# Optimization experiments

Measured on AMD Instinct MI355X. Metric: run time of the kernel, lower is better.

Reference implementation:

```python
import jax, jax.numpy as jnp
import numpy as np

N_NODES = 100000
N_EDGES = 1600000
IN_FEATS = 128
HEADS = 4
OUT_FEATS = 16
NEG_SLOPE = 0.2  # DGL GATConv default negative_slope


def setup_inputs() -> dict:
    key = jax.random.key(0)
    ks = jax.random.split(key, 7)
    feats = jax.random.normal(ks[0], (N_NODES, IN_FEATS), dtype=jnp.float32)
    W = jax.random.normal(ks[1], (HEADS * OUT_FEATS, IN_FEATS), dtype=jnp.float32) * 0.05
    attn_l = jax.random.normal(ks[2], (HEADS, OUT_FEATS), dtype=jnp.float32) * 0.1
    attn_r = jax.random.normal(ks[3], (HEADS, OUT_FEATS), dtype=jnp.float32) * 0.1
    bias = jax.random.normal(ks[4], (HEADS * OUT_FEATS,), dtype=jnp.float32) * 0.01
    src = jax.random.randint(ks[5], (N_EDGES,), 0, N_NODES, dtype=jnp.int64 if jax.config.jax_enable_x64 else jnp.int32)
    dst = jax.random.randint(ks[6], (N_EDGES,), 0, N_NODES, dtype=jnp.int64 if jax.config.jax_enable_x64 else jnp.int32)
    return {"feats": feats, "W": W, "attn_l": attn_l, "attn_r": attn_r,
            "bias": bias, "src": src, "dst": dst}


def reference(feats, W, attn_l, attn_r, bias, src, dst):
    """GATConv forward on a homogeneous graph built from concatenated edge lists.

    feats: [N, in_feats]; W: [H*F, in_feats]; attn_l/attn_r: [H, F]; bias: [H*F]
    src/dst: [E] edge endpoint indices. Returns [N, H, F] (DGL GATConv output).
    """
    N = feats.shape[0]
    H, F = attn_l.shape
    # Linear projection, per-head split: z [N, H, F]
    z = (feats @ W.T).reshape(N, H, F)
    # Per-node attention logits: el/er [N, H]
    el = jnp.einsum('nhf,hf->nh', z, attn_l)
    er = jnp.einsum('nhf,hf->nh', z, attn_r)
    # Per-edge unnormalized attention: e [E, H]
    e = jax.nn.leaky_relu(el[src] + er[dst], negative_slope=NEG_SLOPE)
    # Edge softmax over incoming edges of each destination node
    m = jax.ops.segment_max(e, dst, num_segments=N)           # [N, H]
    m = jnp.where(jnp.isfinite(m), m, jnp.zeros_like(m))      # guard empty segments
    ex = jnp.exp(e - m[dst])                                  # [E, H]
    denom = jax.ops.segment_sum(ex, dst, num_segments=N)      # [N, H]
    alpha = ex / denom[dst]                                   # [E, H]
    # Weighted message aggregation: scatter-add z[src] * alpha into dst
    msg = z[src] * alpha[:, :, None]                          # [E, H, F]
    out = jax.ops.segment_sum(msg, dst, num_segments=N)       # [N, H, F]
    return out + bias.reshape(1, H, F)
```

## Files before the change

### kernel.cpp

```cpp
#include <hip/hip_runtime.h>

#define N_NODES 100000
#define N_EDGES 1600000
#define IN_F    128
#define HEADS   4
#define OUT_F   16
#define HF      64
#define NEG_SLOPE 0.2f

#define BUCK    112
#define NBUCK   893
#define BSTRIDE 2048

#define BSC_CHUNK 4096
#define NB_BSC5 391

#define NB_MFMA2 782
#define NB_FUSED5 1173

typedef __attribute__((ext_vector_type(8))) short short8;
typedef __attribute__((ext_vector_type(4))) float f32x4;

__device__ __forceinline__ short f2bf(float f) {
    union { float f; unsigned u; } v; v.f = f;
    return (short)((v.u + 0x7FFFu + ((v.u >> 16) & 1u)) >> 16);
}

__global__ __launch_bounds__(256) void k_prep(const float* __restrict__ W,
                                              const float* __restrict__ attn_l,
                                              const float* __restrict__ attn_r,
                                              unsigned short* __restrict__ Wfrag,
                                              int* __restrict__ gcur) {
    const int g = blockIdx.x, t = threadIdx.x;
    if (g >= 20) {
        int i = (g - 20) * 256 + t;
        if (i < 1024) gcur[i] = 0;
        return;
    }
    const int ct = g >> 2, kf = g & 3;
    #pragma unroll
    for (int e = 0; e < 2; ++e) {
        int off = e * 256 + t;
        int j = off & 7, lane = off >> 3;
        int n = lane & 15, qq = lane >> 4;
        int k = kf * 32 + qq * 8 + j;
        float v;
        if (ct < 4) {
            v = W[(size_t)(ct * 16 + n) * IN_F + k];
        } else if (n < 8) {
            int hh = n & 3;
            const float* at = (n < 4) ? attn_l : attn_r;
            v = 0.f;
            #pragma unroll
            for (int f = 0; f < 16; ++f)
                v += W[(size_t)(hh * 16 + f) * IN_F + k] * at[hh * 16 + f];
        } else {
            v = 0.f;
        }
        Wfrag[(size_t)g * 512 + off] = (unsigned short)f2bf(v);
    }
}

__global__ __launch_bounds__(512) void k_fused(const float* __restrict__ feats,
                                               const unsigned short* __restrict__ Wfrag,
                                               unsigned short* __restrict__ zb,
                                               float* __restrict__ el,
                                               float* __restrict__ er,
                                               const int* __restrict__ src,
                                               const int* __restrict__ dst,
                                               int* __restrict__ gcur,
                                               unsigned* __restrict__ bin) {
    const int t = threadIdx.x;
    const unsigned bx = blockIdx.x;
    const unsigned q3 = bx / 3u, r3 = bx % 3u;

    if (r3 == 0u) {
        __shared__ unsigned sortedL[BSC_CHUNK];
        __shared__ int hist[NBUCK];
        __shared__ int cur[NBUCK];

        const int bid = (int)q3;
        const int start = bid * BSC_CHUNK;
        int end = start + BSC_CHUNK;
        if (end > N_EDGES) end = N_EDGES;

        for (int i = t; i < NBUCK; i += 512) hist[i] = 0;
        __syncthreads();

        unsigned myv[8];
        #pragma unroll
        for (int k = 0; k < 8; ++k) {
            int i = start + t + k * 512;
            if (i < end) {
                unsigned d = (unsigned)dst[i];
                unsigned b = d / BUCK;
                myv[k] = (b << 7) | (d - b * BUCK);
                atomicAdd(&hist[b], 1);
            } else myv[k] = 0xFFFFFFFFu;
        }
        __syncthreads();

        if (t < 64) {
            int base = t * 14;
            int loc[14]; int acc = 0;
            #pragma unroll
            for (int k = 0; k < 14; ++k) {
                int idx = base + k;
                int v = (idx < NBUCK) ? hist[idx] : 0;
                loc[k] = acc; acc += v;
            }
            int x = acc;
            #pragma unroll
            for (int o = 1; o < 64; o <<= 1) {
                int y = __shfl_up(x, o);
                if (t >= o) x += y;
            }
            int excl = x - acc;
            #pragma unroll
            for (int k = 0; k < 14; ++k) {
                int idx = base + k;
                if (idx < NBUCK) cur[idx] = excl + loc[k];
            }
        }
        __syncthreads();

        #pragma unroll
        for (int k = 0; k < 8; ++k) {
            if (myv[k] != 0xFFFFFFFFu) {
                int i = start + t + k * 512;
                unsigned b = myv[k] >> 7;
                unsigned dl = myv[k] & 127u;
                int pos = atomicAdd(&cur[b], 1);
                sortedL[pos] = (unsigned)src[i] | (dl << 17);
            }
        }
        __syncthreads();

        for (int b = t; b < NBUCK; b += 512) {
            int n = hist[b];
            if (!n) continue;
            int lo = cur[b] - n;
            int gb = atomicAdd(&gcur[b], n);
            unsigned* dp = bin + (size_t)b * BSTRIDE;
            for (int k2 = 0; k2 < n; ++k2) {
                int gpos = gb + k2;
                if (gpos < BSTRIDE) dp[gpos] = sortedL[lo + k2];
            }
        }
        return;
    }

    const int bid = (int)(q3 * 2u + (r3 - 1u));

    const int grp = t >> 6;
    const int l = t & 63;
    const int q = l >> 4, n = l & 15;

    short8 bfrag[5][4];
    #pragma unroll
    for (int ct = 0; ct < 5; ++ct)
        #pragma unroll
        for (int kf = 0; kf < 4; ++kf)
            bfrag[ct][kf] = *(const short8*)(Wfrag + (size_t)((ct * 4 + kf) * 64 + l) * 8);

    int anode = bid * 128 + grp * 16 + n;
    int aclamp = anode < N_NODES ? anode : 0;
    const float* arow = feats + (size_t)aclamp * IN_F + q * 8;

    f32x4 acc[5];
    #pragma unroll
    for (int ct = 0; ct < 5; ++ct) acc[ct] = (f32x4){0.f, 0.f, 0.f, 0.f};

    #pragma unroll
    for (int kf = 0; kf < 4; ++kf) {
        float4 x = *(const float4*)(arow + kf * 32);
        float4 y = *(const float4*)(arow + kf * 32 + 4);
        short8 a;
        a[0] = f2bf(x.x); a[1] = f2bf(x.y); a[2] = f2bf(x.z); a[3] = f2bf(x.w);
        a[4] = f2bf(y.x); a[5] = f2bf(y.y); a[6] = f2bf(y.z); a[7] = f2bf(y.w);
        #pragma unroll
        for (int ct = 0; ct < 5; ++ct)
            acc[ct] = __builtin_amdgcn_mfma_f32_16x16x32_bf16(a, bfrag[ct][kf], acc[ct], 0, 0, 0);
    }

    #pragma unroll
    for (int reg = 0; reg < 4; ++reg) {
        int onode = bid * 128 + grp * 16 + q * 4 + reg;
        if (onode >= N_NODES) continue;
        #pragma unroll
        for (int ct = 0; ct < 4; ++ct)
            zb[(size_t)onode * HF + ct * 16 + n] = (unsigned short)f2bf(acc[ct][reg]);
        float v4 = acc[4][reg];
        if (n < 4)       el[onode * HEADS + n] = v4;
        else if (n < 8)  er[onode * HEADS + (n - 4)] = v4;
    }
}

__global__ __launch_bounds__(512) void k3_sort(const unsigned* __restrict__ bin,
                                               const int* __restrict__ gcur,
                                               const float* __restrict__ el,
                                               const float* __restrict__ er,
                                               const unsigned short* __restrict__ zb,
                                               const float* __restrict__ bias,
                                               float* __restrict__ out) {
    __shared__ unsigned raw[BSTRIDE];
    __shared__ unsigned sorted[BSTRIDE];
    __shared__ int hist[BUCK];
    __shared__ int noff[BUCK + 1];
    __shared__ int cur[BUCK];
    __shared__ int s[128];
    __shared__ float er_s[BUCK * HEADS];

    const int t = threadIdx.x;
    const int B = blockIdx.x;
    const int nodebase = B * BUCK;
    const unsigned* mybin = bin + (size_t)B * BSTRIDE;
    int cnt = gcur[B];
    if (cnt > BSTRIDE) cnt = BSTRIDE;

    if (t < BUCK) hist[t] = 0;
    if (t < BUCK * HEADS) {
        int g = nodebase * HEADS + t;
        er_s[t] = (g < N_NODES * HEADS) ? er[g] : 0.f;
    }
    for (int i = t; i < cnt; i += 512) raw[i] = mybin[i];
    __syncthreads();

    for (int i = t; i < cnt; i += 512)
        atomicAdd(&hist[raw[i] >> 17], 1);
    __syncthreads();

    if (t < 128) s[t] = (t < BUCK) ? hist[t] : 0;
    __syncthreads();
    for (int o = 1; o < 128; o <<= 1) {
        int x = (t < 128 && t >= o) ? s[t - o] : 0;
        __syncthreads();
        if (t < 128) s[t] += x;
        __syncthreads();
    }
    if (t < BUCK) {
        int excl = s[t] - hist[t];
        noff[t] = excl;
        cur[t] = excl;
    }
    if (t == 0) noff[BUCK] = s[BUCK - 1];
    __syncthreads();

    for (int i = t; i < cnt; i += 512) {
        unsigned p = raw[i];
        int pos = atomicAdd(&cur[p >> 17], 1);
        sorted[pos] = p & 0x1FFFF;
    }
    __syncthreads();

    const int wave = t >> 6, lane = t & 63;
    const int j = lane >> 3;
    const int c = lane & 7;
    const int h = c >> 1;
    const int jj = j & 3;
    const int sel = j >> 2;

    for (int p = wave; p < BUCK / 2; p += 8) {
        const int nl = p * 2 + sel;
        const int node = nodebase + nl;
        const int nlo = noff[nl], nhi = noff[nl + 1];
        const float er_d = er_s[nl * HEADS + h];

        float4 A0 = make_float4(0.f, 0.f, 0.f, 0.f);
        float4 A1 = make_float4(0.f, 0.f, 0.f, 0.f);
        float den = 0.f;
        for (int i = nlo + jj; i < nhi; i += 4) {
            int sN = (int)sorted[i];
            float x = el[sN * HEADS + h] + er_d;
            x = x > 0.f ? x : NEG_SLOPE * x;
            float ex = __expf(x);
            den += ex;
            uint4 v = *(const uint4*)(zb + (size_t)sN * HF + c * 8);
            A0.x += ex * __uint_as_float(v.x << 16);
            A0.y += ex * __uint_as_float(v.x & 0xFFFF0000u);
            A0.z += ex * __uint_as_float(v.y << 16);
            A0.w += ex * __uint_as_float(v.y & 0xFFFF0000u);
            A1.x += ex * __uint_as_float(v.z << 16);
            A1.y += ex * __uint_as_float(v.z & 0xFFFF0000u);
            A1.z += ex * __uint_as_float(v.w << 16);
            A1.w += ex * __uint_as_float(v.w & 0xFFFF0000u);
        }
        #pragma unroll
        for (int m = 8; m <= 16; m <<= 1) {
            A0.x += __shfl_xor(A0.x, m); A0.y += __shfl_xor(A0.y, m);
            A0.z += __shfl_xor(A0.z, m); A0.w += __shfl_xor(A0.w, m);
            A1.x += __shfl_xor(A1.x, m); A1.y += __shfl_xor(A1.y, m);
            A1.z += __shfl_xor(A1.z, m); A1.w += __shfl_xor(A1.w, m);
            den  += __shfl_xor(den,  m);
        }
        if (jj == 0 && node < N_NODES) {
            float4 b0 = *(const float4*)(bias + c * 8);
            float4 b1 = *(const float4*)(bias + c * 8 + 4);
            if (den > 0.f) {
                float inv = 1.f / den;
                b0.x += A0.x * inv; b0.y += A0.y * inv;
                b0.z += A0.z * inv; b0.w += A0.w * inv;
                b1.x += A1.x * inv; b1.y += A1.y * inv;
                b1.z += A1.z * inv; b1.w += A1.w * inv;
            }
            *(float4*)(out + (size_t)node * HF + c * 8) = b0;
            *(float4*)(out + (size_t)node * HF + c * 8 + 4) = b1;
        }
    }
}

extern "C" void kernel_launch(void* const* d_in, const int* in_sizes, int n_in,
                              void* d_out, int out_size, void* d_ws, size_t ws_size,
                              hipStream_t stream) {
    const float* feats  = (const float*)d_in[0];
    const float* W      = (const float*)d_in[1];
    const float* attn_l = (const float*)d_in[2];
    const float* attn_r = (const float*)d_in[3];
    const float* bias   = (const float*)d_in[4];
    const int*   src    = (const int*)d_in[5];
    const int*   dst    = (const int*)d_in[6];
    float* out = (float*)d_out;

    char* ws = (char*)d_ws;
    unsigned short* zb = (unsigned short*)ws;  ws += (size_t)N_NODES * HF * 2;
    float* el    = (float*)ws;                 ws += N_NODES * HEADS * 4;
    float* er    = (float*)ws;                 ws += N_NODES * HEADS * 4;
    unsigned short* Wfrag = (unsigned short*)ws; ws += 20 * 64 * 8 * 2;
    int*   gcur  = (int*)ws;                   ws += 1024 * 4;
    unsigned* bin = (unsigned*)ws;             ws += (size_t)NBUCK * BSTRIDE * 4;

    k_prep  <<<24,         256,  0, stream>>>(W, attn_l, attn_r, Wfrag, gcur);
    k_fused <<<NB_FUSED5,  512,  0, stream>>>(feats, Wfrag, zb, el, er, src, dst, gcur, bin);
    k3_sort <<<NBUCK,      512,  0, stream>>>(bin, gcur, el, er, zb, bias, out);
}
```

Measured before the change: 171.4 us.

## Split z into head-half planes and process each bucket in two head-split blocks

```diff
diff --git a/kernel.cpp b/kernel.cpp
--- a/kernel.cpp
+++ b/kernel.cpp
@@ -17,6 +17,8 @@
 
 #define NB_MFMA2 782
 #define NB_FUSED5 1173
+
+#define K3H_BLOCKS 1792
 
 typedef __attribute__((ext_vector_type(8))) short short8;
 typedef __attribute__((ext_vector_type(4))) float f32x4;
@@ -63,7 +65,7 @@
 
 __global__ __launch_bounds__(512) void k_fused(const float* __restrict__ feats,
                                                const unsigned short* __restrict__ Wfrag,
-                                               unsigned short* __restrict__ zb,
+                                               unsigned short* __restrict__ zbh,
                                                float* __restrict__ el,
                                                float* __restrict__ er,
                                                const int* __restrict__ src,
@@ -189,7 +191,8 @@
         if (onode >= N_NODES) continue;
         #pragma unroll
         for (int ct = 0; ct < 4; ++ct)
-            zb[(size_t)onode * HF + ct * 16 + n] = (unsigned short)f2bf(acc[ct][reg]);
+            zbh[((size_t)(ct >> 1) * N_NODES + onode) * 32 + (ct & 1) * 16 + n] =
+                (unsigned short)f2bf(acc[ct][reg]);
         float v4 = acc[4][reg];
         if (n < 4)       el[onode * HEADS + n] = v4;
         else if (n < 8)  er[onode * HEADS + (n - 4)] = v4;
@@ -200,7 +203,7 @@
                                                const int* __restrict__ gcur,
                                                const float* __restrict__ el,
                                                const float* __restrict__ er,
-                                               const unsigned short* __restrict__ zb,
+                                               const unsigned short* __restrict__ zbh,
                                                const float* __restrict__ bias,
                                                float* __restrict__ out) {
     __shared__ unsigned raw[BSTRIDE];
@@ -209,19 +212,22 @@
     __shared__ int noff[BUCK + 1];
     __shared__ int cur[BUCK];
     __shared__ int s[128];
-    __shared__ float er_s[BUCK * HEADS];
+    __shared__ float er_s[BUCK * 2];
 
     const int t = threadIdx.x;
-    const int B = blockIdx.x;
+    const unsigned bx = blockIdx.x;
+    const int half = (int)((bx & 7u) >> 2);
+    const int B = (int)((bx >> 3) * 4u + (bx & 3u));
+    if (B >= NBUCK) return;
     const int nodebase = B * BUCK;
     const unsigned* mybin = bin + (size_t)B * BSTRIDE;
     int cnt = gcur[B];
     if (cnt > BSTRIDE) cnt = BSTRIDE;
 
     if (t < BUCK) hist[t] = 0;
-    if (t < BUCK * HEADS) {
-        int g = nodebase * HEADS + t;
-        er_s[t] = (g < N_NODES * HEADS) ? er[g] : 0.f;
+    if (t < BUCK * 2) {
+        int node = nodebase + (t >> 1);
+        er_s[t] = (node < N_NODES) ? er[node * HEADS + half * 2 + (t & 1)] : 0.f;
     }
     for (int i = t; i < cnt; i += 512) raw[i] = mybin[i];
     __syncthreads();
@@ -254,28 +260,31 @@
     __syncthreads();
 
     const int wave = t >> 6, lane = t & 63;
-    const int j = lane >> 3;
-    const int c = lane & 7;
-    const int h = c >> 1;
+    const int j = lane >> 2;
+    const int c4 = lane & 3;
+    const int hl = c4 >> 1;
     const int jj = j & 3;
     const int sel = j >> 2;
 
-    for (int p = wave; p < BUCK / 2; p += 8) {
-        const int nl = p * 2 + sel;
+    const unsigned short* zhalf = zbh + (size_t)half * N_NODES * 32;
+    const int hglob = half * 2 + hl;
+
+    for (int p = wave; p < BUCK / 4; p += 8) {
+        const int nl = p * 4 + sel;
         const int node = nodebase + nl;
         const int nlo = noff[nl], nhi = noff[nl + 1];
-        const float er_d = er_s[nl * HEADS + h];
+        const float er_d = er_s[nl * 2 + hl];
 
         float4 A0 = make_float4(0.f, 0.f, 0.f, 0.f);
         float4 A1 = make_float4(0.f, 0.f, 0.f, 0.f);
         float den = 0.f;
         for (int i = nlo + jj; i < nhi; i += 4) {
             int sN = (int)sorted[i];
-            float x = el[sN * HEADS + h] + er_d;
+            float x = el[sN * HEADS + hglob] + er_d;
             x = x > 0.f ? x : NEG_SLOPE * x;
             float ex = __expf(x);
             den += ex;
-            uint4 v = *(const uint4*)(zb + (size_t)sN * HF + c * 8);
+            uint4 v = *(const uint4*)(zhalf + (size_t)sN * 32 + c4 * 8);
             A0.x += ex * __uint_as_float(v.x << 16);
             A0.y += ex * __uint_as_float(v.x & 0xFFFF0000u);
             A0.z += ex * __uint_as_float(v.y << 16);
@@ -286,7 +295,7 @@
             A1.w += ex * __uint_as_float(v.w & 0xFFFF0000u);
         }
         #pragma unroll
-        for (int m = 8; m <= 16; m <<= 1) {
+        for (int m = 4; m <= 8; m <<= 1) {
             A0.x += __shfl_xor(A0.x, m); A0.y += __shfl_xor(A0.y, m);
             A0.z += __shfl_xor(A0.z, m); A0.w += __shfl_xor(A0.w, m);
             A1.x += __shfl_xor(A1.x, m); A1.y += __shfl_xor(A1.y, m);
@@ -294,8 +303,8 @@
             den  += __shfl_xor(den,  m);
         }
         if (jj == 0 && node < N_NODES) {
-            float4 b0 = *(const float4*)(bias + c * 8);
-            float4 b1 = *(const float4*)(bias + c * 8 + 4);
+            float4 b0 = *(const float4*)(bias + half * 32 + c4 * 8);
+            float4 b1 = *(const float4*)(bias + half * 32 + c4 * 8 + 4);
             if (den > 0.f) {
                 float inv = 1.f / den;
                 b0.x += A0.x * inv; b0.y += A0.y * inv;
@@ -303,8 +312,8 @@
                 b1.x += A1.x * inv; b1.y += A1.y * inv;
                 b1.z += A1.z * inv; b1.w += A1.w * inv;
             }
-            *(float4*)(out + (size_t)node * HF + c * 8) = b0;
-            *(float4*)(out + (size_t)node * HF + c * 8 + 4) = b1;
+            *(float4*)(out + (size_t)node * HF + half * 32 + c4 * 8) = b0;
+            *(float4*)(out + (size_t)node * HF + half * 32 + c4 * 8 + 4) = b1;
         }
     }
 }
@@ -322,7 +331,7 @@
     float* out = (float*)d_out;
 
     char* ws = (char*)d_ws;
-    unsigned short* zb = (unsigned short*)ws;  ws += (size_t)N_NODES * HF * 2;
+    unsigned short* zbh = (unsigned short*)ws; ws += (size_t)N_NODES * HF * 2;
     float* el    = (float*)ws;                 ws += N_NODES * HEADS * 4;
     float* er    = (float*)ws;                 ws += N_NODES * HEADS * 4;
     unsigned short* Wfrag = (unsigned short*)ws; ws += 20 * 64 * 8 * 2;
@@ -330,6 +339,6 @@
     unsigned* bin = (unsigned*)ws;             ws += (size_t)NBUCK * BSTRIDE * 4;
 
     k_prep  <<<24,         256,  0, stream>>>(W, attn_l, attn_r, Wfrag, gcur);
-    k_fused <<<NB_FUSED5,  512,  0, stream>>>(feats, Wfrag, zb, el, er, src, dst, gcur, bin);
-    k3_sort <<<NBUCK,      512,  0, stream>>>(bin, gcur, el, er, zb, bias, out);
-}
+    k_fused <<<NB_FUSED5,  512,  0, stream>>>(feats, Wfrag, zbh, el, er, src, dst, gcur, bin);
+    k3_sort <<<K3H_BLOCKS, 512,  0, stream>>>(bin, gcur, el, er, zbh, bias, out);
+}
```

Measured after the change: 182.0 us. +6.2%, slower.
